# Kernel optimization log

Hardware: AMD Instinct MI355X
Metric: run time of the kernel (lower is better)

The kernel has to match this reference:

```python
import jax, jax.numpy as jnp
import numpy as np

N_NODES = 50000
N_EDGES = 800000
N_GRAPHS = 512
IN_DIM, HID_DIM, EMB_DIM = 128, 256, 128
EPS = 1e-5


def setup_inputs() -> dict:
    key = jax.random.key(0)
    ks = jax.random.split(key, 12)
    x = jax.random.normal(ks[0], (N_NODES, IN_DIM), dtype=jnp.float32)
    edge_index = jax.random.randint(ks[1], (2, N_EDGES), 0, N_NODES, dtype=jnp.int32)
    batch = jnp.sort(jax.random.randint(ks[2], (N_NODES,), 0, N_GRAPHS, dtype=jnp.int32))
    s1 = 1.0 / np.sqrt(IN_DIM)
    s2 = 1.0 / np.sqrt(HID_DIM)
    return {
        "x": x,
        "edge_index": edge_index,
        "batch": batch,
        "W1": jax.random.uniform(ks[3], (IN_DIM, HID_DIM), jnp.float32, -s1, s1),
        "b1": jnp.zeros((HID_DIM,), jnp.float32),
        "gamma1": jnp.ones((HID_DIM,), jnp.float32),
        "beta1": jnp.zeros((HID_DIM,), jnp.float32),
        "W2": jax.random.uniform(ks[4], (HID_DIM, EMB_DIM), jnp.float32, -s2, s2),
        "b2": jnp.zeros((EMB_DIM,), jnp.float32),
        "gamma2": jnp.ones((EMB_DIM,), jnp.float32),
        "beta2": jnp.zeros((EMB_DIM,), jnp.float32),
    }


def _gcn_conv(x, W, b, src, dst, n_nodes):
    # PyG GCNConv: h = xW; aggregate with sym-normalized adjacency incl. self-loops; + bias
    h = x @ W  # [N, D]
    ones = jnp.ones(src.shape[0], dtype=h.dtype)
    deg = jax.ops.segment_sum(ones, dst, num_segments=n_nodes) + 1.0  # self-loop
    dinv = jax.lax.rsqrt(deg)
    norm = dinv[src] * dinv[dst]  # [E]
    msg = h[src] * norm[:, None]  # gather + scale  [E, D]
    agg = jax.ops.segment_sum(msg, dst, num_segments=n_nodes)
    agg = agg + h * (1.0 / deg)[:, None]  # self-loop contribution (norm = 1/deg)
    return agg + b


def _batchnorm(h, gamma, beta):
    mean = jnp.mean(h, axis=0)
    var = jnp.mean(jnp.square(h - mean), axis=0)  # biased, training mode
    return gamma * (h - mean) * jax.lax.rsqrt(var + EPS) + beta


def reference(x, edge_index, batch, W1, b1, gamma1, beta1, W2, b2, gamma2, beta2):
    src, dst = edge_index[0], edge_index[1]
    n = x.shape[0]
    h = _gcn_conv(x, W1, b1, src, dst, n)
    h = _batchnorm(jax.nn.relu(h), gamma1, beta1)
    h = _gcn_conv(h, W2, b2, src, dst, n)
    h = _batchnorm(jax.nn.relu(h), gamma2, beta2)
    return jax.ops.segment_max(h, batch, num_segments=N_GRAPHS)
```

## Files before the change

### kernel.cpp

```cpp
#include <hip/hip_runtime.h>
#include <math.h>

#define N_NODES 50000
#define N_EDGES 800000
#define N_GRAPHS 512
#define IN_DIM 128
#define HID_DIM 256
#define EMB_DIM 128
#define EPS 1e-5f
#define ELLW 64
#define NV4 (N_EDGES / 4)
#define NB 196
#define CAP 8192
#define PA_BLOCKS 512
#define CPB ((NV4 + PA_BLOCKS - 1) / PA_BLOCKS)
#define F2B_N (N_NODES * IN_DIM / 4)
#define F2B_BLOCKS ((F2B_N + 255) / 256)
#define TW1_BLOCKS ((HID_DIM * IN_DIM + 255) / 256)
#define NSLOTS 128
#define GSLOTS 128

typedef __attribute__((ext_vector_type(8))) short bf16x8;
typedef __attribute__((ext_vector_type(4))) float f32x4;
typedef __attribute__((ext_vector_type(4))) int i32x4;
typedef __attribute__((ext_vector_type(4))) unsigned short u16x4;

static __device__ __forceinline__ unsigned short f2b(float f) {
    unsigned u = __float_as_uint(f);
    return (unsigned short)((u + 0x7fffu + ((u >> 16) & 1u)) >> 16);
}
static __device__ __forceinline__ float dinv_of(int d) {
    return rsqrtf((float)(min(d, ELLW) + 1));
}

__global__ void __launch_bounds__(256) scatter_convert(const int* __restrict__ src,
                                                       const int* __restrict__ dst,
                                                       int* __restrict__ gcur,
                                                       int* __restrict__ bucketbuf,
                                                       const float* __restrict__ x,
                                                       unsigned short* __restrict__ xbf,
                                                       const float* __restrict__ W1,
                                                       unsigned short* __restrict__ W1t) {
    int b = blockIdx.x;
    if (b < PA_BLOCKS) {
        __shared__ int hcnt[NB], hbase[NB], loff[NB];
        int t = threadIdx.x;
        for (int j = t; j < NB; j += 256) { hcnt[j] = 0; loff[j] = 0; }
        __syncthreads();
        int base = b * CPB;
        int i_end = min(base + CPB, NV4);
        const i32x4* dst4 = (const i32x4*)dst;
        const i32x4* src4 = (const i32x4*)src;
        int i0 = base + t, i1 = base + 256 + t;
        bool val0 = i0 < i_end, val1 = i1 < i_end;
        i32x4 d0 = {0, 0, 0, 0}, s0 = {0, 0, 0, 0};
        i32x4 d1 = {0, 0, 0, 0}, s1 = {0, 0, 0, 0};
        if (val0) {
            d0 = __builtin_nontemporal_load(&dst4[i0]);
            s0 = __builtin_nontemporal_load(&src4[i0]);
        }
        if (val1) {
            d1 = __builtin_nontemporal_load(&dst4[i1]);
            s1 = __builtin_nontemporal_load(&src4[i1]);
        }
        if (val0) {
#pragma unroll
            for (int e = 0; e < 4; ++e) atomicAdd(&hcnt[d0[e] >> 8], 1);
        }
        if (val1) {
#pragma unroll
            for (int e = 0; e < 4; ++e) atomicAdd(&hcnt[d1[e] >> 8], 1);
        }
        __syncthreads();
        for (int j = t; j < NB; j += 256) {
            int c = hcnt[j];
            if (c) hbase[j] = atomicAdd(&gcur[j], c);
        }
        __syncthreads();
        if (val0) {
#pragma unroll
            for (int e = 0; e < 4; ++e) {
                int d = d0[e], bk = d >> 8;
                int o = atomicAdd(&loff[bk], 1);
                int idx = hbase[bk] + o;
                if (idx < CAP) bucketbuf[bk * CAP + idx] = ((d & 255) << 16) | s0[e];
            }
        }
        if (val1) {
#pragma unroll
            for (int e = 0; e < 4; ++e) {
                int d = d1[e], bk = d >> 8;
                int o = atomicAdd(&loff[bk], 1);
                int idx = hbase[bk] + o;
                if (idx < CAP) bucketbuf[bk * CAP + idx] = ((d & 255) << 16) | s1[e];
            }
        }
    } else if (b < PA_BLOCKS + F2B_BLOCKS) {
        int i = (b - PA_BLOCKS) * 256 + threadIdx.x;
        if (i < F2B_N) {
            f32x4 v = __builtin_nontemporal_load(&((const f32x4*)x)[i]);
            u16x4 o;
            o[0] = f2b(v[0]); o[1] = f2b(v[1]); o[2] = f2b(v[2]); o[3] = f2b(v[3]);
            __builtin_nontemporal_store(o, &((u16x4*)xbf)[i]);
        }
    } else {
        int j = (b - PA_BLOCKS - F2B_BLOCKS) * 256 + threadIdx.x;
        if (j < HID_DIM * IN_DIM) {
            int n = j >> 7;
            int k = j & 127;
            W1t[j] = f2b(W1[k * HID_DIM + n]);
        }
    }
}

__global__ void __launch_bounds__(256) build_ell(const int* __restrict__ gcur,
                                                 const int* __restrict__ bucketbuf,
                                                 int* __restrict__ fill,
                                                 int* __restrict__ col) {
    __shared__ unsigned short lcol[256 * ELLW];
    __shared__ int lfill[256];
    int b = blockIdx.x;
    int t = threadIdx.x;
    lfill[t] = 0;
    __syncthreads();
    int n = min(gcur[b], CAP);
    const int* buf = bucketbuf + b * CAP;
    for (int i = t; i < n; i += 256) {
        int p = buf[i];
        int dl = p >> 16;
        int pos = atomicAdd(&lfill[dl], 1);
        if (pos < ELLW) lcol[(dl << 6) + pos] = (unsigned short)(p & 0xFFFF);
    }
    __syncthreads();
    int v = (b << 8) + t;
    if (v < N_NODES) fill[v] = lfill[t];
    for (int idx4 = t; idx4 < 256 * (ELLW / 4); idx4 += 256) {
        int row = idx4 >> 4;
        int vv = (b << 8) + row;
        if (vv < N_NODES) {
            int c0 = (idx4 & 15) << 2;
            u16x4 w = *(const u16x4*)&lcol[(row << 6) + c0];
            int4 o4 = make_int4(w[0], w[1], w[2], w[3]);
            *(int4*)&col[((size_t)vv << 6) + c0] = o4;
        }
    }
}

static __device__ __forceinline__ void acc8(float* acc, uint4 r, float w) {
    const unsigned* u = (const unsigned*)&r;
#pragma unroll
    for (int k = 0; k < 4; ++k) {
        float lo = __uint_as_float((u[k] & 0xFFFFu) << 16);
        float hi = __uint_as_float(u[k] & 0xFFFF0000u);
        acc[2 * k]     += w * lo;
        acc[2 * k + 1] += w * hi;
    }
}

template <bool RELU, bool OUT_BF, bool BIAS, bool STATS>
__global__ void __launch_bounds__(256) aggw_kernel(const unsigned short* __restrict__ h,
                                                   const int* __restrict__ deg,
                                                   const int* __restrict__ col,
                                                   const float* __restrict__ bias,
                                                   void* __restrict__ y,
                                                   float* __restrict__ sumP,
                                                   float* __restrict__ sqP) {
    __shared__ float sv[STATS ? 16 : 1][STATS ? 128 : 1];
    int tid = threadIdx.x;
    int lane = tid & 63;
    int grpw = lane >> 4;
    int p = lane & 15;
    int grp = tid >> 4;
    int v = blockIdx.x * 16 + grp;

    int dcl = min(deg[v], ELLW);
    uint4 selfr = *(const uint4*)(h + (size_t)v * 128 + p * 8);

    float acc[8] = {};
    int sl = grpw << 4;
#pragma unroll 4
    for (int sel = 0; sel < 4; ++sel) {
        int base = sel * 16;
        if (base >= dcl) break;
        int idx = base + p;
        int cidx = min(idx, dcl - 1);
        int u_l = col[(v << 6) + cidx];
        float w_l = (idx < dcl) ? dinv_of(deg[u_l]) : 0.f;
        int n = min(16, dcl - base);
        for (int e0 = 0; e0 < n; e0 += 4) {
            int u0 = __shfl(u_l, sl + e0, 64);
            int u1 = __shfl(u_l, sl + e0 + 1, 64);
            int u2 = __shfl(u_l, sl + e0 + 2, 64);
            int u3 = __shfl(u_l, sl + e0 + 3, 64);
            float w0 = __shfl(w_l, sl + e0, 64);
            float w1 = __shfl(w_l, sl + e0 + 1, 64);
            float w2 = __shfl(w_l, sl + e0 + 2, 64);
            float w3 = __shfl(w_l, sl + e0 + 3, 64);
            uint4 d0 = *(const uint4*)(h + (size_t)u0 * 128 + p * 8);
            uint4 d1 = *(const uint4*)(h + (size_t)u1 * 128 + p * 8);
            uint4 d2 = *(const uint4*)(h + (size_t)u2 * 128 + p * 8);
            uint4 d3 = *(const uint4*)(h + (size_t)u3 * 128 + p * 8);
            acc8(acc, d0, w0);
            acc8(acc, d1, w1);
            acc8(acc, d2, w2);
            acc8(acc, d3, w3);
        }
    }

    {
        const unsigned* su = (const unsigned*)&selfr;
        float dv = rsqrtf((float)(dcl + 1));
        float dv2 = dv * dv;
        float o[8];
#pragma unroll
        for (int k = 0; k < 4; ++k) {
            float lo = __uint_as_float((su[k] & 0xFFFFu) << 16);
            float hi = __uint_as_float(su[k] & 0xFFFF0000u);
            o[2 * k]     = dv * acc[2 * k]     + lo * dv2;
            o[2 * k + 1] = dv * acc[2 * k + 1] + hi * dv2;
        }
        if (BIAS) {
            float4 bv0 = *(const float4*)&bias[p * 8];
            float4 bv1 = *(const float4*)&bias[p * 8 + 4];
            o[0] += bv0.x; o[1] += bv0.y; o[2] += bv0.z; o[3] += bv0.w;
            o[4] += bv1.x; o[5] += bv1.y; o[6] += bv1.z; o[7] += bv1.w;
        }
        if (RELU) {
#pragma unroll
            for (int k = 0; k < 8; ++k) o[k] = fmaxf(o[k], 0.f);
        }
        if (OUT_BF) {
            uint4 packed;
            unsigned* pu = (unsigned*)&packed;
#pragma unroll
            for (int k = 0; k < 4; ++k)
                pu[k] = (unsigned)f2b(o[2 * k]) | ((unsigned)f2b(o[2 * k + 1]) << 16);
            *(uint4*)((unsigned short*)y + (size_t)v * 128 + p * 8) = packed;
        } else {
            float* yf = (float*)y + (size_t)v * 128 + p * 8;
            *(float4*)yf = make_float4(o[0], o[1], o[2], o[3]);
            *(float4*)(yf + 4) = make_float4(o[4], o[5], o[6], o[7]);
        }
        if (STATS) {
#pragma unroll
            for (int k = 0; k < 8; ++k) sv[grp][p * 8 + k] = o[k];
        }
    }

    if (STATS) {
        __syncthreads();
        if (tid < 128) {
            float s = 0.f, q = 0.f;
#pragma unroll
            for (int r = 0; r < 16; ++r) {
                float val = sv[r][tid];
                s += val;
                q += val * val;
            }
            int slot = blockIdx.x & (NSLOTS - 1);
            atomicAdd(&sumP[slot * 128 + tid], s);
            atomicAdd(&sqP[slot * 128 + tid], q);
        }
    }
}

template <bool RELU, bool STATS>
__global__ void __launch_bounds__(256) mfma_gemm_kernel(const unsigned short* __restrict__ A,
                                                        const unsigned short* __restrict__ Bt,
                                                        const float* __restrict__ bias,
                                                        unsigned short* __restrict__ C,
                                                        float* __restrict__ sums,
                                                        float* __restrict__ sumsqs,
                                                        int M, int N, int K) {
    const int LDT = 40;
    __shared__ unsigned short As[64 * LDT];
    __shared__ unsigned short Bs[64 * LDT];
    int tid = threadIdx.x;
    int bm = blockIdx.x * 64;
    int bn = blockIdx.y * 64;
    int lr = tid >> 2;
    int lc = (tid & 3) * 8;
    int lane = tid & 63;
    int w = tid >> 6;
    int wr = (w >> 1) * 32, wc = (w & 1) * 32;
    int l15 = lane & 15, q = lane >> 4;

    f32x4 acc[2][2] = {};
    bool arow_ok = (bm + lr) < M;
    const unsigned short* Aptr = A + (size_t)(bm + lr) * K + lc;
    const unsigned short* Bptr = Bt + (size_t)(bn + lr) * K + lc;

    uint4 av = arow_ok ? *(const uint4*)(Aptr) : make_uint4(0u, 0u, 0u, 0u);
    uint4 bv = *(const uint4*)(Bptr);

    for (int k0 = 0; k0 < K; k0 += 32) {
        *(uint4*)&As[lr * LDT + lc] = av;
        *(uint4*)&Bs[lr * LDT + lc] = bv;
        __syncthreads();
        if (k0 + 32 < K) {
            av = arow_ok ? *(const uint4*)(Aptr + k0 + 32) : make_uint4(0u, 0u, 0u, 0u);
            bv = *(const uint4*)(Bptr + k0 + 32);
        }
        bf16x8 a0 = *(const bf16x8*)&As[(wr + 0 + l15) * LDT + q * 8];
        bf16x8 a1 = *(const bf16x8*)&As[(wr + 16 + l15) * LDT + q * 8];
        bf16x8 b0 = *(const bf16x8*)&Bs[(wc + 0 + l15) * LDT + q * 8];
        bf16x8 b1 = *(const bf16x8*)&Bs[(wc + 16 + l15) * LDT + q * 8];
        acc[0][0] = __builtin_amdgcn_mfma_f32_16x16x32_bf16(a0, b0, acc[0][0], 0, 0, 0);
        acc[0][1] = __builtin_amdgcn_mfma_f32_16x16x32_bf16(a0, b1, acc[0][1], 0, 0, 0);
        acc[1][0] = __builtin_amdgcn_mfma_f32_16x16x32_bf16(a1, b0, acc[1][0], 0, 0, 0);
        acc[1][1] = __builtin_amdgcn_mfma_f32_16x16x32_bf16(a1, b1, acc[1][1], 0, 0, 0);
        __syncthreads();
    }

    float scol[2] = {0.f, 0.f};
    float qcol[2] = {0.f, 0.f};
#pragma unroll
    for (int mi = 0; mi < 2; ++mi)
#pragma unroll
        for (int ni = 0; ni < 2; ++ni) {
            int colc = bn + wc + ni * 16 + l15;
            float bv2 = bias ? bias[colc] : 0.f;
#pragma unroll
            for (int r = 0; r < 4; ++r) {
                int row = bm + wr + mi * 16 + q * 4 + r;
                if (row < M) {
                    float vv = acc[mi][ni][r] + bv2;
                    if (RELU) vv = fmaxf(vv, 0.f);
                    C[(size_t)row * N + colc] = f2b(vv);
                    if (STATS) { scol[ni] += vv; qcol[ni] += vv * vv; }
                }
            }
        }

    if (STATS) {
        __shared__ float sred[4][2][16];
        __shared__ float qred[4][2][16];
#pragma unroll
        for (int ni = 0; ni < 2; ++ni) {
            float s = scol[ni], qq = qcol[ni];
            s += __shfl_xor(s, 16, 64);
            s += __shfl_xor(s, 32, 64);
            qq += __shfl_xor(qq, 16, 64);
            qq += __shfl_xor(qq, 32, 64);
            if (lane < 16) { sred[w][ni][l15] = s; qred[w][ni][l15] = qq; }
        }
        __syncthreads();
        if (tid < 64) {
            int par = (tid >> 5) & 1;
            int ni = (tid >> 4) & 1;
            int l = tid & 15;
            int slot = blockIdx.x & (GSLOTS - 1);
            atomicAdd(&sums[slot * HID_DIM + bn + tid],
                      sred[par][ni][l] + sred[par + 2][ni][l]);
            atomicAdd(&sumsqs[slot * HID_DIM + bn + tid],
                      qred[par][ni][l] + qred[par + 2][ni][l]);
        }
    }
}

__global__ void __launch_bounds__(256) prep2_kernel(const float* __restrict__ sum1P,
                                                    const float* __restrict__ sumsq1P,
                                                    const float* __restrict__ gamma1,
                                                    const float* __restrict__ beta1,
                                                    const float* __restrict__ W2,
                                                    unsigned short* __restrict__ W2pt,
                                                    float* __restrict__ bc2) {
    __shared__ float a1s[HID_DIM], s1s[HID_DIM];
    __shared__ float bp[16][17];
    int t = threadIdx.x;
    {
        float s = 0.f, q = 0.f;
#pragma unroll 8
        for (int j = 0; j < GSLOTS; ++j) {
            s += sum1P[j * HID_DIM + t];
            q += sumsq1P[j * HID_DIM + t];
        }
        float m = s * (1.f / N_NODES);
        float var = q * (1.f / N_NODES) - m * m;
        float a = gamma1[t] * rsqrtf(var + EPS);
        a1s[t] = a;
        s1s[t] = beta1[t] - m * a;
    }
    __syncthreads();
    int row = blockIdx.x * 16 + (t & 15);
    int ks = t >> 4;
    float bacc = 0.f;
    unsigned short wloc[16];
#pragma unroll
    for (int j = 0; j < 16; ++j) {
        int k = ks * 16 + j;
        float wv = W2[k * EMB_DIM + row];
        wloc[j] = f2b(a1s[k] * wv);
        bacc += s1s[k] * wv;
    }
    *(uint4*)&W2pt[(size_t)row * HID_DIM + ks * 16]     = *(uint4*)&wloc[0];
    *(uint4*)&W2pt[(size_t)row * HID_DIM + ks * 16 + 8] = *(uint4*)&wloc[8];
    bp[t & 15][ks] = bacc;
    __syncthreads();
    if (t < 16) {
        float s = 0.f;
#pragma unroll
        for (int g = 0; g < 16; ++g) s += bp[t][g];
        bc2[blockIdx.x * 16 + t] = s;
    }
}

__global__ void __launch_bounds__(128) segmax_kernel(const float* __restrict__ y,
                                                     const float* __restrict__ sumP,
                                                     const float* __restrict__ sqP,
                                                     const float* __restrict__ gamma2,
                                                     const float* __restrict__ beta2,
                                                     const int* __restrict__ batch,
                                                     float* __restrict__ out) {
    __shared__ int sh[2];
    int g = blockIdx.x;
    int c = threadIdx.x;
    float s2 = 0.f, q2 = 0.f;
#pragma unroll 8
    for (int j = 0; j < NSLOTS; ++j) {
        s2 += sumP[j * 128 + c];
        q2 += sqP[j * 128 + c];
    }
    float mch = s2 * (1.f / N_NODES);
    float var = q2 * (1.f / N_NODES) - mch * mch;
    float ac = gamma2[c] * rsqrtf(var + EPS);
    float sc = beta2[c] - mch * ac;
    if (threadIdx.x == 0) {
        int lo = 0, hi = N_NODES;
        while (lo < hi) { int mid = (lo + hi) >> 1; if (batch[mid] < g) lo = mid + 1; else hi = mid; }
        sh[0] = lo;
        hi = N_NODES;
        while (lo < hi) { int mid = (lo + hi) >> 1; if (batch[mid] < g + 1) lo = mid + 1; else hi = mid; }
        sh[1] = lo;
    }
    __syncthreads();
    int beg = sh[0], end = sh[1];
    float m = -INFINITY;
    for (int v = beg; v < end; ++v) {
        m = fmaxf(m, fmaf(ac, y[(size_t)v * EMB_DIM + c], sc));
    }
    out[(size_t)g * EMB_DIM + c] = m;
}

extern "C" void kernel_launch(void* const* d_in, const int* in_sizes, int n_in,
                              void* d_out, int out_size, void* d_ws, size_t ws_size,
                              hipStream_t stream) {
    const float* x      = (const float*)d_in[0];
    const int*   ei     = (const int*)d_in[1];
    const int*   batch  = (const int*)d_in[2];
    const float* W1     = (const float*)d_in[3];
    const float* b1     = (const float*)d_in[4];
    const float* gamma1 = (const float*)d_in[5];
    const float* beta1  = (const float*)d_in[6];
    const float* W2     = (const float*)d_in[7];
    const float* b2     = (const float*)d_in[8];
    const float* gamma2 = (const float*)d_in[9];
    const float* beta2  = (const float*)d_in[10];
    float* out = (float*)d_out;

    char* ws = (char*)d_ws;
    size_t off = 0;
    auto alloc = [&](size_t bytes) -> char* {
        char* p = ws + off;
        off = (off + bytes + 255) & ~(size_t)255;
        return p;
    };
    int*   gcur    = (int*)alloc((size_t)NB * 4);
    float* gsumP   = (float*)alloc((size_t)GSLOTS * HID_DIM * 4);
    float* gsqP    = (float*)alloc((size_t)GSLOTS * HID_DIM * 4);
    float* sumP    = (float*)alloc((size_t)NSLOTS * 128 * 4);
    float* sqP     = (float*)alloc((size_t)NSLOTS * 128 * 4);
    size_t zbytes = off;
    int*   fill   = (int*)alloc((size_t)N_NODES * 4);
    int*   bucketbuf = (int*)alloc((size_t)NB * CAP * 4);
    int*   col    = (int*)alloc((size_t)N_NODES * ELLW * 4);
    float* bc2    = (float*)alloc((size_t)EMB_DIM * 4);
    unsigned short* W1t  = (unsigned short*)alloc((size_t)HID_DIM * IN_DIM * 2);
    unsigned short* W2pt = (unsigned short*)alloc((size_t)HID_DIM * EMB_DIM * 2);
    unsigned short* xbf  = (unsigned short*)alloc((size_t)N_NODES * IN_DIM * 2);
    unsigned short* axbf = (unsigned short*)alloc((size_t)N_NODES * IN_DIM * 2);
    unsigned short* y1bf = (unsigned short*)alloc((size_t)N_NODES * HID_DIM * 2);
    unsigned short* gbf  = (unsigned short*)alloc((size_t)N_NODES * EMB_DIM * 2);
    float* y2 = (float*)xbf;
    (void)ws_size; (void)in_sizes; (void)n_in; (void)out_size;

    const int* src  = ei;
    const int* dstp = ei + N_EDGES;

    hipMemsetAsync(ws, 0, zbytes, stream);

    scatter_convert<<<PA_BLOCKS + F2B_BLOCKS + TW1_BLOCKS, 256, 0, stream>>>(
        src, dstp, gcur, bucketbuf, x, xbf, W1, W1t);
    build_ell<<<NB, 256, 0, stream>>>(gcur, bucketbuf, fill, col);

    aggw_kernel<false, true, false, false><<<N_NODES / 16, 256, 0, stream>>>(
        xbf, fill, col, nullptr, axbf, nullptr, nullptr);
    dim3 g1((N_NODES + 63) / 64, HID_DIM / 64);
    mfma_gemm_kernel<true, true><<<g1, 256, 0, stream>>>(axbf, W1t, b1, y1bf,
                                                         gsumP, gsqP,
                                                         N_NODES, HID_DIM, IN_DIM);

    prep2_kernel<<<8, 256, 0, stream>>>(gsumP, gsqP, gamma1, beta1, W2, W2pt, bc2);

    dim3 g2((N_NODES + 63) / 64, EMB_DIM / 64);
    mfma_gemm_kernel<false, false><<<g2, 256, 0, stream>>>(y1bf, W2pt, bc2, gbf,
                                                           nullptr, nullptr,
                                                           N_NODES, EMB_DIM, HID_DIM);
    aggw_kernel<true, false, true, true><<<N_NODES / 16, 256, 0, stream>>>(
        gbf, fill, col, b2, y2, sumP, sqP);

    segmax_kernel<<<N_GRAPHS, 128, 0, stream>>>(y2, sumP, sqP,
                                                gamma2, beta2, batch, out);
}
```

Baseline: 259.1 us.

## Fuse first-layer neighbor aggregation with W1 GEMM, bias, ReLU and BN stats

New measurement: 264.5 us. 1.02x slower.

```diff
diff --git a/kernel.cpp b/kernel.cpp
--- a/kernel.cpp
+++ b/kernel.cpp
@@ -19,6 +19,7 @@
 #define TW1_BLOCKS ((HID_DIM * IN_DIM + 255) / 256)
 #define NSLOTS 128
 #define GSLOTS 128
+#define AG_BLOCKS ((N_NODES + 63) / 64)
 
 typedef __attribute__((ext_vector_type(8))) short bf16x8;
 typedef __attribute__((ext_vector_type(4))) float f32x4;
@@ -154,6 +155,142 @@
         float hi = __uint_as_float(u[k] & 0xFFFF0000u);
         acc[2 * k]     += w * lo;
         acc[2 * k + 1] += w * hi;
+    }
+}
+
+__global__ void __launch_bounds__(256) fused_aggemm1(const unsigned short* __restrict__ xbf,
+                                                     const int* __restrict__ deg,
+                                                     const int* __restrict__ col,
+                                                     const unsigned short* __restrict__ W1t,
+                                                     const float* __restrict__ bias,
+                                                     unsigned short* __restrict__ y1,
+                                                     float* __restrict__ sums,
+                                                     float* __restrict__ sumsqs) {
+    const int LDA = 136;
+    __shared__ unsigned short As[64 * LDA];
+    __shared__ float sred[4][2][16];
+    __shared__ float qred[4][2][16];
+    int tid = threadIdx.x;
+    int lane = tid & 63;
+    int w = tid >> 6;
+    int grpw = lane >> 4;
+    int p = lane & 15;
+    int grp = tid >> 4;
+    int bm = blockIdx.x * 64;
+    int sl = grpw << 4;
+
+#pragma unroll
+    for (int it = 0; it < 4; ++it) {
+        int vl = grp + (it << 4);
+        int v = bm + vl;
+        float o[8] = {};
+        if (v < N_NODES) {
+            int dcl = min(deg[v], ELLW);
+            uint4 selfr = *(const uint4*)(xbf + (size_t)v * 128 + p * 8);
+            float acc[8] = {};
+            for (int sel = 0; sel < 4; ++sel) {
+                int base = sel * 16;
+                if (base >= dcl) break;
+                int idx = base + p;
+                int cidx = min(idx, dcl - 1);
+                int u_l = col[((size_t)v << 6) + cidx];
+                float w_l = (idx < dcl) ? dinv_of(deg[u_l]) : 0.f;
+                int n = min(16, dcl - base);
+                for (int e0 = 0; e0 < n; e0 += 4) {
+                    int u0 = __shfl(u_l, sl + e0, 64);
+                    int u1 = __shfl(u_l, sl + e0 + 1, 64);
+                    int u2 = __shfl(u_l, sl + e0 + 2, 64);
+                    int u3 = __shfl(u_l, sl + e0 + 3, 64);
+                    float w0 = __shfl(w_l, sl + e0, 64);
+                    float w1 = __shfl(w_l, sl + e0 + 1, 64);
+                    float w2 = __shfl(w_l, sl + e0 + 2, 64);
+                    float w3 = __shfl(w_l, sl + e0 + 3, 64);
+                    uint4 d0 = *(const uint4*)(xbf + (size_t)u0 * 128 + p * 8);
+                    uint4 d1 = *(const uint4*)(xbf + (size_t)u1 * 128 + p * 8);
+                    uint4 d2 = *(const uint4*)(xbf + (size_t)u2 * 128 + p * 8);
+                    uint4 d3 = *(const uint4*)(xbf + (size_t)u3 * 128 + p * 8);
+                    acc8(acc, d0, w0);
+                    acc8(acc, d1, w1);
+                    acc8(acc, d2, w2);
+                    acc8(acc, d3, w3);
+                }
+            }
+            const unsigned* su = (const unsigned*)&selfr;
+            float dv = rsqrtf((float)(dcl + 1));
+            float dv2 = dv * dv;
+#pragma unroll
+            for (int k = 0; k < 4; ++k) {
+                float lo = __uint_as_float((su[k] & 0xFFFFu) << 16);
+                float hi = __uint_as_float(su[k] & 0xFFFF0000u);
+                o[2 * k]     = dv * acc[2 * k]     + lo * dv2;
+                o[2 * k + 1] = dv * acc[2 * k + 1] + hi * dv2;
+            }
+        }
+        uint4 packed;
+        unsigned* pu = (unsigned*)&packed;
+#pragma unroll
+        for (int k = 0; k < 4; ++k)
+            pu[k] = (unsigned)f2b(o[2 * k]) | ((unsigned)f2b(o[2 * k + 1]) << 16);
+        *(uint4*)&As[vl * LDA + p * 8] = packed;
+    }
+    __syncthreads();
+
+    int wr = (w >> 1) * 32, wc = (w & 1) * 32;
+    int l15 = lane & 15, q = lane >> 4;
+    for (int s = 0; s < 4; ++s) {
+        f32x4 acc2[2][2] = {};
+        const unsigned short* Bbase = W1t + (size_t)(s * 64 + wc) * 128;
+#pragma unroll
+        for (int k0 = 0; k0 < 128; k0 += 32) {
+            bf16x8 a0 = *(const bf16x8*)&As[(wr + 0 + l15) * LDA + k0 + q * 8];
+            bf16x8 a1 = *(const bf16x8*)&As[(wr + 16 + l15) * LDA + k0 + q * 8];
+            bf16x8 b0 = *(const bf16x8*)(Bbase + (size_t)(0 + l15) * 128 + k0 + q * 8);
+            bf16x8 b1 = *(const bf16x8*)(Bbase + (size_t)(16 + l15) * 128 + k0 + q * 8);
+            acc2[0][0] = __builtin_amdgcn_mfma_f32_16x16x32_bf16(a0, b0, acc2[0][0], 0, 0, 0);
+            acc2[0][1] = __builtin_amdgcn_mfma_f32_16x16x32_bf16(a0, b1, acc2[0][1], 0, 0, 0);
+            acc2[1][0] = __builtin_amdgcn_mfma_f32_16x16x32_bf16(a1, b0, acc2[1][0], 0, 0, 0);
+            acc2[1][1] = __builtin_amdgcn_mfma_f32_16x16x32_bf16(a1, b1, acc2[1][1], 0, 0, 0);
+        }
+        float scol[2] = {0.f, 0.f};
+        float qcol[2] = {0.f, 0.f};
+#pragma unroll
+        for (int mi = 0; mi < 2; ++mi)
+#pragma unroll
+            for (int ni = 0; ni < 2; ++ni) {
+                int colc = s * 64 + wc + ni * 16 + l15;
+                float bv = bias[colc];
+#pragma unroll
+                for (int r = 0; r < 4; ++r) {
+                    int row = bm + wr + mi * 16 + q * 4 + r;
+                    if (row < N_NODES) {
+                        float vv = acc2[mi][ni][r] + bv;
+                        vv = fmaxf(vv, 0.f);
+                        y1[(size_t)row * HID_DIM + colc] = f2b(vv);
+                        scol[ni] += vv; qcol[ni] += vv * vv;
+                    }
+                }
+            }
+#pragma unroll
+        for (int ni = 0; ni < 2; ++ni) {
+            float ss = scol[ni], qq = qcol[ni];
+            ss += __shfl_xor(ss, 16, 64);
+            ss += __shfl_xor(ss, 32, 64);
+            qq += __shfl_xor(qq, 16, 64);
+            qq += __shfl_xor(qq, 32, 64);
+            if (lane < 16) { sred[w][ni][l15] = ss; qred[w][ni][l15] = qq; }
+        }
+        __syncthreads();
+        if (tid < 64) {
+            int par = (tid >> 5) & 1;
+            int ni = (tid >> 4) & 1;
+            int l = tid & 15;
+            int slot = blockIdx.x & (GSLOTS - 1);
+            atomicAdd(&sums[slot * HID_DIM + s * 64 + tid],
+                      sred[par][ni][l] + sred[par + 2][ni][l]);
+            atomicAdd(&sumsqs[slot * HID_DIM + s * 64 + tid],
+                      qred[par][ni][l] + qred[par + 2][ni][l]);
+        }
+        __syncthreads();
     }
 }
 
@@ -312,8 +449,6 @@
         __syncthreads();
     }
 
-    float scol[2] = {0.f, 0.f};
-    float qcol[2] = {0.f, 0.f};
 #pragma unroll
     for (int mi = 0; mi < 2; ++mi)
 #pragma unroll
@@ -327,35 +462,9 @@
                     float vv = acc[mi][ni][r] + bv2;
                     if (RELU) vv = fmaxf(vv, 0.f);
                     C[(size_t)row * N + colc] = f2b(vv);
-                    if (STATS) { scol[ni] += vv; qcol[ni] += vv * vv; }
                 }
             }
         }
-
-    if (STATS) {
-        __shared__ float sred[4][2][16];
-        __shared__ float qred[4][2][16];
-#pragma unroll
-        for (int ni = 0; ni < 2; ++ni) {
-            float s = scol[ni], qq = qcol[ni];
-            s += __shfl_xor(s, 16, 64);
-            s += __shfl_xor(s, 32, 64);
-            qq += __shfl_xor(qq, 16, 64);
-            qq += __shfl_xor(qq, 32, 64);
-            if (lane < 16) { sred[w][ni][l15] = s; qred[w][ni][l15] = qq; }
-        }
-        __syncthreads();
-        if (tid < 64) {
-            int par = (tid >> 5) & 1;
-            int ni = (tid >> 4) & 1;
-            int l = tid & 15;
-            int slot = blockIdx.x & (GSLOTS - 1);
-            atomicAdd(&sums[slot * HID_DIM + bn + tid],
-                      sred[par][ni][l] + sred[par + 2][ni][l]);
-            atomicAdd(&sumsqs[slot * HID_DIM + bn + tid],
-                      qred[par][ni][l] + qred[par + 2][ni][l]);
-        }
-    }
 }
 
 __global__ void __launch_bounds__(256) prep2_kernel(const float* __restrict__ sum1P,
@@ -478,7 +587,6 @@
     unsigned short* W1t  = (unsigned short*)alloc((size_t)HID_DIM * IN_DIM * 2);
     unsigned short* W2pt = (unsigned short*)alloc((size_t)HID_DIM * EMB_DIM * 2);
     unsigned short* xbf  = (unsigned short*)alloc((size_t)N_NODES * IN_DIM * 2);
-    unsigned short* axbf = (unsigned short*)alloc((size_t)N_NODES * IN_DIM * 2);
     unsigned short* y1bf = (unsigned short*)alloc((size_t)N_NODES * HID_DIM * 2);
     unsigned short* gbf  = (unsigned short*)alloc((size_t)N_NODES * EMB_DIM * 2);
     float* y2 = (float*)xbf;
@@ -493,12 +601,8 @@
         src, dstp, gcur, bucketbuf, x, xbf, W1, W1t);
     build_ell<<<NB, 256, 0, stream>>>(gcur, bucketbuf, fill, col);
 
-    aggw_kernel<false, true, false, false><<<N_NODES / 16, 256, 0, stream>>>(
-        xbf, fill, col, nullptr, axbf, nullptr, nullptr);
-    dim3 g1((N_NODES + 63) / 64, HID_DIM / 64);
-    mfma_gemm_kernel<true, true><<<g1, 256, 0, stream>>>(axbf, W1t, b1, y1bf,
-                                                         gsumP, gsqP,
-                                                         N_NODES, HID_DIM, IN_DIM);
+    fused_aggemm1<<<AG_BLOCKS, 256, 0, stream>>>(xbf, fill, col, W1t, b1, y1bf,
+                                                 gsumP, gsqP);
 
     prep2_kernel<<<8, 256, 0, stream>>>(gsumP, gsqP, gamma1, beta1, W2, W2pt, bc2);
 
```
